# Optimization experiments

Hardware: AMD Instinct MI355X
Metric: run time of the kernel (lower is better)

The kernel has to match this reference:

```python
import jax, jax.numpy as jnp
import numpy as np

RATE = 22050.0 / 256.0  # audio_target_rate from the torch source
SIZES = [2.23147392 * RATE, 2.62519274 * RATE, 3.74199546 * RATE,
         5.78800454 * RATE, 8.02371882 * RATE, float('inf')]
WEIGHT = 1.0
EPS = 1e-7


def _giou_1d(a, b):
    # a, b: [P, 2] intervals (start, end); elementwise 1-D GIoU
    inter = jnp.clip(jnp.minimum(a[:, 1], b[:, 1]) - jnp.maximum(a[:, 0], b[:, 0]), 0.0)
    union = (a[:, 1] - a[:, 0]) + (b[:, 1] - b[:, 0]) - inter
    iou = inter / (union + EPS)
    enclose = jnp.maximum(a[:, 1], b[:, 1]) - jnp.minimum(a[:, 0], b[:, 0])
    return iou - (enclose - union) / (enclose + EPS)


def setup_inputs() -> dict:
    key = jax.random.key(0)
    ks = jax.random.split(key, 4)
    B, N = 4, 32
    L0 = 131072  # frames at the finest level
    levels = 6
    anchors = {f"anchors_l{i}": (jnp.arange(L0 >> i, dtype=jnp.float32) + 0.5) * (2.0 ** i)
               for i in range(levels)}
    A = sum(int(v.shape[0]) for v in anchors.values())  # 258048
    # GT intervals: all rows belong to class 0 (matches class_id filter in the source)
    starts = jax.random.uniform(ks[0], (B, N), minval=0.0, maxval=float(L0) - 2000.0)
    lens = jax.random.uniform(ks[1], (B, N), minval=50.0, maxval=1500.0)
    annotations = jnp.stack([starts, starts + lens, jnp.zeros((B, N))], axis=-1).astype(jnp.float32)
    # Predicted intervals for every anchor
    c = jax.random.uniform(ks[2], (B, A), minval=0.0, maxval=float(L0))
    w = jax.random.uniform(ks[3], (B, A), minval=10.0, maxval=2000.0)
    regressions = jnp.stack([c - 0.5 * w, c + 0.5 * w], axis=-1).astype(jnp.float32)
    out = {"regressions": regressions, "annotations": annotations, "class_id": 0}
    out.update(anchors)
    return out


def reference(regressions, annotations, anchors_l0, anchors_l1, anchors_l2,
              anchors_l3, anchors_l4, anchors_l5, class_id):
    anchors_list = [anchors_l0, anchors_l1, anchors_l2, anchors_l3, anchors_l4, anchors_l5]
    all_pts = jnp.concatenate(anchors_list)  # [A]

    def per_sample(reg, ann):
        # ann: [N, 3]; inputs guarantee every row has class == class_id and is valid
        order = jnp.argsort(ann[:, 1] - ann[:, 0])  # sort GT by length ascending
        ann = ann[order]
        s, e = ann[:, 0:1], ann[:, 1:2]  # [N,1]
        pos_parts, nl_parts, nr_parts = [], [], []
        for i, pts in enumerate(anchors_list):
            l = pts[None, :] - s            # [N, A_i]
            r = e - pts[None, :]            # [N, A_i]
            in_gt = (l >= 0.0) & (r >= 0.0)
            m = jnp.maximum(l, r)
            lower = SIZES[i - 1] if i > 0 else 0.0
            cand = in_gt & (m >= lower) & (m < SIZES[i])
            pos_parts.append(cand.any(axis=0))
            amax = jnp.argmax(cand, axis=0)  # first True per anchor (0 if none)
            inv = 1.0 / (2.0 ** i)           # normalize l*/r* by 2**level
            nl_parts.append(jnp.take_along_axis(l, amax[None, :], axis=0)[0] * inv)
            nr_parts.append(jnp.take_along_axis(r, amax[None, :], axis=0)[0] * inv)
        pos = jnp.concatenate(pos_parts)   # [A] bool
        nl = jnp.concatenate(nl_parts)     # [A]
        nr = jnp.concatenate(nr_parts)     # [A]
        # decoded normalized target boxes around the anchor points
        boxes = jnp.stack([all_pts - nl, all_pts + nr], axis=1)  # [A, 2]
        giou = jnp.clip(_giou_1d(boxes, reg[:, :2]), -1.0, 1.0)
        loss = 1.0 - giou
        posf = pos.astype(loss.dtype)
        # masked mean over positive anchors (torch indexes by boolean mask then .mean())
        return jnp.sum(loss * posf) / jnp.maximum(jnp.sum(posf), 1.0) * WEIGHT

    return jax.vmap(per_sample)(regressions, annotations)  # [B] per-sample losses
```

## Files before the change

kernel.cpp:

```cpp
#include <hip/hip_runtime.h>

#define EPS_F 1e-7f
#define NN 32
#define MARGIN 3
#define NSEG (NN * 6)
#define TPB 1024
#define CHUNK 4
#define CAND_MAX 24576

__global__ __launch_bounds__(TPB) void rl_fused(
    const float* __restrict__ reg,
    const float* __restrict__ ann,
    int c0, int A,
    float* __restrict__ out)
{
    const int b = blockIdx.x;
    const int t = threadIdx.x;
    const int wave = t >> 6;
    const int lane = t & 63;

    __shared__ float2 sh_se[NN];
    __shared__ int4   seg[NSEG];
    __shared__ int    pfx[NSEG];
    __shared__ unsigned segmask[NSEG];
    __shared__ unsigned cand32[CAND_MAX / 4];
    __shared__ float  sh_sz[8];
    __shared__ float  red_l[TPB / 64], red_p[TPB / 64];

    if (t < 8) {
        const float szc[8] = {
            0.0f,
            (float)(2.23147392 * (22050.0 / 256.0)),
            (float)(2.62519274 * (22050.0 / 256.0)),
            (float)(3.74199546 * (22050.0 / 256.0)),
            (float)(5.78800454 * (22050.0 / 256.0)),
            (float)(8.02371882 * (22050.0 / 256.0)),
            __builtin_inff(), __builtin_inff()
        };
        sh_sz[t] = szc[t];
    }

    if (t < NN) {
        const float* an = ann + (size_t)b * (size_t)NN * 3;
        const float s0 = an[t * 3 + 0];
        const float e0 = an[t * 3 + 1];
        const float len = e0 - s0;
        int rank = 0;
#pragma unroll
        for (int j = 0; j < NN; ++j) {
            const float lj = __shfl(len, j, 64);
            rank += (lj < len) || (lj == len && j < t);
        }
        sh_se[rank] = make_float2(s0, e0);
    }
    __syncthreads();

    float tsx, tsy;
    {
        const float2 tmp = sh_se[lane & 31];
        tsx = tmp.x; tsy = tmp.y;
    }

    if (t < NSEG) {
        const int n   = t / 6;
        const int lvl = t - n * 6;
        const float2 se = sh_se[n];
        const float s = se.x, e = se.y;
        const float mid   = 0.5f * (s + e);
        const float halfL = 0.5f * (e - s);
        const float lo = sh_sz[lvl];
        const float hi = sh_sz[lvl + 1];
        const int   cnt = c0 >> lvl;
        const float inv   = __int_as_float((127 - lvl) << 23);
        const float scale = __int_as_float((127 + lvl) << 23);

        const float dlo = fmaxf(lo - halfL, 0.0f);
        const float dhi = hi - halfL;
        const float prl = fmaxf(mid + dlo, s);
        const float prh = fminf(mid + dhi, e);
        const float pll = fmaxf(mid - dhi, s);
        const float plh = fminf(mid - dlo, e);

        int r0 = (int)floorf(prl * inv - 0.5f) - MARGIN;
        int r1 = (int)floorf(prh * inv - 0.5f) + MARGIN;
        int l0 = (int)floorf(pll * inv - 0.5f) - MARGIN;
        int l1 = (int)floorf(plh * inv - 0.5f) + MARGIN;
        r0 = max(r0, 0); r1 = min(r1, cnt - 1);
        l0 = max(l0, 0); l1 = min(l1, cnt - 1);
        if (r1 >= r0) l1 = min(l1, r0 - 1);
        const int lenL = max(l1 - l0 + 1, 0);
        const int lenR = max(r1 - r0 + 1, 0);
        seg[t] = make_int4(l0, r0, lenL | (lenR << 16), (n << 8) | lvl);
        pfx[t] = lenL + lenR;

        const int firstloc = lenL ? l0 : r0;
        const int lastloc  = lenR ? r1 : l1;
        const float ptmin = ((float)firstloc + 0.5f) * scale;
        const float ptmax = ((float)lastloc  + 0.5f) * scale;
        unsigned msk = 0u;
#pragma unroll
        for (int n2 = 0; n2 < NN - 1; ++n2) {
            const float ox = __shfl(tsx, n2, 64);
            const float oy = __shfl(tsy, n2, 64);
            msk |= ((n2 < n) & (ox <= ptmax) & (oy >= ptmin)) ? (1u << n2) : 0u;
        }
        segmask[t] = msk;
    }
    __syncthreads();

    if (wave == 0) {
        int carry = 0;
#pragma unroll
        for (int k = 0; k < 3; ++k) {
            int v = pfx[k * 64 + lane];
#pragma unroll
            for (int o = 1; o < 64; o <<= 1) {
                const int u = __shfl_up(v, o, 64);
                v += (lane >= o) ? u : 0;
            }
            pfx[k * 64 + lane] = v + carry;
            carry += __shfl(v, 63, 64);
        }
    }
    __syncthreads();
    const int T = min(pfx[NSEG - 1], CAND_MAX);

    if (t < NSEG) {
        const int4 sg = seg[t];
        const int count = (sg.z & 0xffff) + (sg.z >> 16);
        const int start = pfx[t] - count;
        seg[t].w = sg.w | (start << 16);
        unsigned char* cbw = (unsigned char*)cand32;
        int i = start;
        const int end = min(start + count, CAND_MAX);
        const unsigned rep = 0x01010101u * (unsigned)t;
        while (i < end && (i & 3)) cbw[i++] = (unsigned char)t;
        for (; i + 4 <= end; i += 4) cand32[i >> 2] = rep;
        for (; i < end; ++i) cbw[i] = (unsigned char)t;
    }
    __syncthreads();

    const int twoc0 = 2 * c0;
    const unsigned char* cb = (const unsigned char*)cand32;
    const float2* reg2 = (const float2*)reg + (size_t)b * A;
    float loss_sum = 0.0f, pos_sum = 0.0f;

    for (int jb = t; jb < T; jb += TPB * CHUNK) {
        float2 gk[CHUNK];
        float  ptk[CHUNK], lk[CHUNK], rk[CHUNK], lok[CHUNK], hik[CHUNK], invk[CHUNK];
        unsigned mskk[CHUNK];
        bool validk[CHUNK];
#pragma unroll
        for (int k = 0; k < CHUNK; ++k) {
            const int j = jb + k * TPB;
            const bool act = j < T;
            const int jj = act ? j : 0;
            const int sid = cb[jj];
            const int4 sg = seg[sid];
            mskk[k] = segmask[sid];
            const int lenL  = sg.z & 0xffff;
            const int start = (int)(((unsigned)sg.w) >> 16);
            const int n     = (sg.w >> 8) & 0xff;
            const int lvl   = sg.w & 0xff;
            const int local = jj - start;
            const int loc = (local < lenL) ? (sg.x + local) : (sg.y + (local - lenL));
            const float scale = __int_as_float((127 + lvl) << 23);
            invk[k] = __int_as_float((127 - lvl) << 23);
            const int aoff = twoc0 - (twoc0 >> lvl);

            gk[k] = reg2[aoff + loc];

            const float pt = ((float)loc + 0.5f) * scale;
            ptk[k] = pt;
            lok[k] = sh_sz[lvl];
            hik[k] = sh_sz[lvl + 1];
            const float2 se = sh_se[n];
            const float l = pt - se.x;
            const float r = se.y - pt;
            lk[k] = l; rk[k] = r;
            const float m = fmaxf(l, r);
            validk[k] = act & (fminf(l, r) >= 0.0f) & (m >= lok[k]) & (m < hik[k]);
        }

#pragma unroll
        for (int k = 0; k < CHUNK; ++k) {
            bool valid = validk[k];
            unsigned msk = mskk[k];
            const float pt = ptk[k];
            const float lo = lok[k], hi = hik[k];
            while (valid && msk) {
                const int n2 = __builtin_ctz(msk);
                msk &= msk - 1u;
                const float2 o = sh_se[n2];
                const float l2 = pt - o.x;
                const float r2 = o.y - pt;
                const float m2 = fmaxf(l2, r2);
                if ((fminf(l2, r2) >= 0.0f) & (m2 >= lo) & (m2 < hi)) valid = false;
            }

            const float inv = invk[k];
            const float2 g = gk[k];
            const float b0 = pt - lk[k] * inv;
            const float b1 = pt + rk[k] * inv;
            const float inter = fmaxf(fminf(b1, g.y) - fmaxf(b0, g.x), 0.0f);
            const float uni = (b1 - b0) + (g.y - g.x) - inter;
            const float iou = inter * __builtin_amdgcn_rcpf(uni + EPS_F);
            const float enc = fmaxf(b1, g.y) - fminf(b0, g.x);
            float giou = iou - (enc - uni) * __builtin_amdgcn_rcpf(enc + EPS_F);
            giou = fminf(fmaxf(giou, -1.0f), 1.0f);
            loss_sum += valid ? (1.0f - giou) : 0.0f;
            pos_sum  += valid ? 1.0f : 0.0f;
        }
    }

    for (int o = 32; o > 0; o >>= 1) {
        loss_sum += __shfl_down(loss_sum, o, 64);
        pos_sum  += __shfl_down(pos_sum,  o, 64);
    }
    if (lane == 0) { red_l[wave] = loss_sum; red_p[wave] = pos_sum; }
    __syncthreads();
    if (t < 16) {
        float Ls = red_l[t];
        float Ps = red_p[t];
#pragma unroll
        for (int o = 8; o > 0; o >>= 1) {
            Ls += __shfl_down(Ls, o, 16);
            Ps += __shfl_down(Ps, o, 16);
        }
        if (t == 0) out[b] = Ls / fmaxf(Ps, 1.0f);
    }
}

extern "C" void kernel_launch(void* const* d_in, const int* in_sizes, int n_in,
                              void* d_out, int out_size, void* d_ws, size_t ws_size,
                              hipStream_t stream) {
    const float* reg = (const float*)d_in[0];
    const float* ann = (const float*)d_in[1];
    const int c0 = in_sizes[3];
    const int A = in_sizes[3] + in_sizes[4] + in_sizes[5] +
                  in_sizes[6] + in_sizes[7] + in_sizes[8];
    const int B = out_size;
    (void)d_ws; (void)ws_size;

    rl_fused<<<dim3(B), TPB, 0, stream>>>(reg, ann, c0, A, (float*)d_out);
}
```

Baseline: 73.94 us.

## Split each sample across multiple blocks with atomic last-block reduction

```diff
diff --git a/kernel.cpp b/kernel.cpp
--- a/kernel.cpp
+++ b/kernel.cpp
@@ -4,17 +4,21 @@
 #define NN 32
 #define MARGIN 3
 #define NSEG (NN * 6)
-#define TPB 1024
+#define TPB 256
+#define SLICES 8
 #define CHUNK 4
 #define CAND_MAX 24576
-
-__global__ __launch_bounds__(TPB) void rl_fused(
+#define CNT_OFF 4096
+
+__global__ __launch_bounds__(TPB) void rl_sliced(
     const float* __restrict__ reg,
     const float* __restrict__ ann,
     int c0, int A,
+    float* __restrict__ ws,
     float* __restrict__ out)
 {
-    const int b = blockIdx.x;
+    const int s_blk = blockIdx.x;
+    const int b = blockIdx.y;
     const int t = threadIdx.x;
     const int wave = t >> 6;
     const int lane = t & 63;
@@ -145,14 +149,14 @@
     const float2* reg2 = (const float2*)reg + (size_t)b * A;
     float loss_sum = 0.0f, pos_sum = 0.0f;
 
-    for (int jb = t; jb < T; jb += TPB * CHUNK) {
+    for (int jb = s_blk * TPB + t; jb < T; jb += SLICES * TPB * CHUNK) {
         float2 gk[CHUNK];
         float  ptk[CHUNK], lk[CHUNK], rk[CHUNK], lok[CHUNK], hik[CHUNK], invk[CHUNK];
         unsigned mskk[CHUNK];
         bool validk[CHUNK];
 #pragma unroll
         for (int k = 0; k < CHUNK; ++k) {
-            const int j = jb + k * TPB;
+            const int j = jb + k * (SLICES * TPB);
             const bool act = j < T;
             const int jj = act ? j : 0;
             const int sid = cb[jj];
@@ -219,15 +223,28 @@
     }
     if (lane == 0) { red_l[wave] = loss_sum; red_p[wave] = pos_sum; }
     __syncthreads();
-    if (t < 16) {
-        float Ls = red_l[t];
-        float Ps = red_p[t];
-#pragma unroll
-        for (int o = 8; o > 0; o >>= 1) {
-            Ls += __shfl_down(Ls, o, 16);
-            Ps += __shfl_down(Ps, o, 16);
-        }
-        if (t == 0) out[b] = Ls / fmaxf(Ps, 1.0f);
+
+    if (t == 0) {
+        float Ls = 0.0f, Ps = 0.0f;
+#pragma unroll
+        for (int w = 0; w < TPB / 64; ++w) { Ls += red_l[w]; Ps += red_p[w]; }
+        float* slot = ws + ((size_t)b * SLICES + s_blk) * 2;
+        atomicExch(&slot[0], Ls);
+        atomicExch(&slot[1], Ps);
+        __threadfence();
+        unsigned* cnt = (unsigned*)((char*)ws + CNT_OFF + (size_t)b * 64);
+        const unsigned old = atomicAdd(cnt, 1u);
+        if (old == SLICES - 1) {
+            __threadfence();
+            float Lt = 0.0f, Pt = 0.0f;
+#pragma unroll
+            for (int i = 0; i < SLICES; ++i) {
+                float* sl = ws + ((size_t)b * SLICES + i) * 2;
+                Lt += atomicAdd(&sl[0], 0.0f);
+                Pt += atomicAdd(&sl[1], 0.0f);
+            }
+            out[b] = Lt / fmaxf(Pt, 1.0f);
+        }
     }
 }
 
@@ -240,7 +257,8 @@
     const int A = in_sizes[3] + in_sizes[4] + in_sizes[5] +
                   in_sizes[6] + in_sizes[7] + in_sizes[8];
     const int B = out_size;
-    (void)d_ws; (void)ws_size;
-
-    rl_fused<<<dim3(B), TPB, 0, stream>>>(reg, ann, c0, A, (float*)d_out);
+
+    hipMemsetAsync(d_ws, 0, 8192, stream);
+    rl_sliced<<<dim3(SLICES, B), TPB, 0, stream>>>(
+        reg, ann, c0, A, (float*)d_ws, (float*)d_out);
 }
```

New measurement: 83.42 us. 12.8% more time.

## Assign one half-wave per GT interval, dropping prefix-scan candidate list

Applied to the files above, without the earlier changes.

```diff
diff --git a/kernel.cpp b/kernel.cpp
--- a/kernel.cpp
+++ b/kernel.cpp
@@ -3,12 +3,10 @@
 #define EPS_F 1e-7f
 #define NN 32
 #define MARGIN 3
-#define NSEG (NN * 6)
 #define TPB 1024
-#define CHUNK 4
-#define CAND_MAX 24576
-
-__global__ __launch_bounds__(TPB) void rl_fused(
+#define CHUNK 2
+
+__global__ __launch_bounds__(TPB) void rl_lean(
     const float* __restrict__ reg,
     const float* __restrict__ ann,
     int c0, int A,
@@ -18,12 +16,10 @@
     const int t = threadIdx.x;
     const int wave = t >> 6;
     const int lane = t & 63;
+    const int n    = t >> 5;
+    const int slot = t & 31;
 
     __shared__ float2 sh_se[NN];
-    __shared__ int4   seg[NSEG];
-    __shared__ int    pfx[NSEG];
-    __shared__ unsigned segmask[NSEG];
-    __shared__ unsigned cand32[CAND_MAX / 4];
     __shared__ float  sh_sz[8];
     __shared__ float  red_l[TPB / 64], red_p[TPB / 64];
 
@@ -55,128 +51,96 @@
     }
     __syncthreads();
 
+    const float2 myse = sh_se[n];
+    const float s = myse.x, e = myse.y;
     float tsx, tsy;
     {
         const float2 tmp = sh_se[lane & 31];
         tsx = tmp.x; tsy = tmp.y;
     }
 
-    if (t < NSEG) {
-        const int n   = t / 6;
-        const int lvl = t - n * 6;
-        const float2 se = sh_se[n];
-        const float s = se.x, e = se.y;
-        const float mid   = 0.5f * (s + e);
-        const float halfL = 0.5f * (e - s);
-        const float lo = sh_sz[lvl];
-        const float hi = sh_sz[lvl + 1];
-        const int   cnt = c0 >> lvl;
-        const float inv   = __int_as_float((127 - lvl) << 23);
-        const float scale = __int_as_float((127 + lvl) << 23);
-
-        const float dlo = fmaxf(lo - halfL, 0.0f);
-        const float dhi = hi - halfL;
-        const float prl = fmaxf(mid + dlo, s);
-        const float prh = fminf(mid + dhi, e);
-        const float pll = fmaxf(mid - dhi, s);
-        const float plh = fminf(mid - dlo, e);
-
-        int r0 = (int)floorf(prl * inv - 0.5f) - MARGIN;
-        int r1 = (int)floorf(prh * inv - 0.5f) + MARGIN;
-        int l0 = (int)floorf(pll * inv - 0.5f) - MARGIN;
-        int l1 = (int)floorf(plh * inv - 0.5f) + MARGIN;
-        r0 = max(r0, 0); r1 = min(r1, cnt - 1);
-        l0 = max(l0, 0); l1 = min(l1, cnt - 1);
-        if (r1 >= r0) l1 = min(l1, r0 - 1);
-        const int lenL = max(l1 - l0 + 1, 0);
-        const int lenR = max(r1 - r0 + 1, 0);
-        seg[t] = make_int4(l0, r0, lenL | (lenR << 16), (n << 8) | lvl);
-        pfx[t] = lenL + lenR;
-
-        const int firstloc = lenL ? l0 : r0;
-        const int lastloc  = lenR ? r1 : l1;
-        const float ptmin = ((float)firstloc + 0.5f) * scale;
-        const float ptmax = ((float)lastloc  + 0.5f) * scale;
-        unsigned msk = 0u;
-#pragma unroll
-        for (int n2 = 0; n2 < NN - 1; ++n2) {
-            const float ox = __shfl(tsx, n2, 64);
-            const float oy = __shfl(tsy, n2, 64);
-            msk |= ((n2 < n) & (ox <= ptmax) & (oy >= ptmin)) ? (1u << n2) : 0u;
-        }
-        segmask[t] = msk;
-    }
-    __syncthreads();
-
-    if (wave == 0) {
-        int carry = 0;
-#pragma unroll
-        for (int k = 0; k < 3; ++k) {
-            int v = pfx[k * 64 + lane];
-#pragma unroll
-            for (int o = 1; o < 64; o <<= 1) {
-                const int u = __shfl_up(v, o, 64);
-                v += (lane >= o) ? u : 0;
-            }
-            pfx[k * 64 + lane] = v + carry;
-            carry += __shfl(v, 63, 64);
-        }
-    }
-    __syncthreads();
-    const int T = min(pfx[NSEG - 1], CAND_MAX);
-
-    if (t < NSEG) {
-        const int4 sg = seg[t];
-        const int count = (sg.z & 0xffff) + (sg.z >> 16);
-        const int start = pfx[t] - count;
-        seg[t].w = sg.w | (start << 16);
-        unsigned char* cbw = (unsigned char*)cand32;
-        int i = start;
-        const int end = min(start + count, CAND_MAX);
-        const unsigned rep = 0x01010101u * (unsigned)t;
-        while (i < end && (i & 3)) cbw[i++] = (unsigned char)t;
-        for (; i + 4 <= end; i += 4) cand32[i >> 2] = rep;
-        for (; i < end; ++i) cbw[i] = (unsigned char)t;
-    }
-    __syncthreads();
+    unsigned msk_gt = 0u;
+#pragma unroll
+    for (int n2 = 0; n2 < NN - 1; ++n2) {
+        const float ox = __shfl(tsx, n2, 64);
+        const float oy = __shfl(tsy, n2, 64);
+        msk_gt |= ((n2 < n) & (ox <= e) & (oy >= s)) ? (1u << n2) : 0u;
+    }
+
+    const float mid   = 0.5f * (s + e);
+    const float halfL = 0.5f * (e - s);
+    int l0a[6], r0a[6], lenLa[6], cumi[6];
+    {
+        int run = 0;
+#pragma unroll
+        for (int lvl = 0; lvl < 6; ++lvl) {
+            const float lo = sh_sz[lvl];
+            const float hi = sh_sz[lvl + 1];
+            const int   cnt = c0 >> lvl;
+            const float inv = __int_as_float((127 - lvl) << 23);
+
+            const float dlo = fmaxf(lo - halfL, 0.0f);
+            const float dhi = hi - halfL;
+            const float prl = fmaxf(mid + dlo, s);
+            const float prh = fminf(mid + dhi, e);
+            const float pll = fmaxf(mid - dhi, s);
+            const float plh = fminf(mid - dlo, e);
+
+            int r0 = (int)floorf(prl * inv - 0.5f) - MARGIN;
+            int r1 = (int)floorf(prh * inv - 0.5f) + MARGIN;
+            int l0 = (int)floorf(pll * inv - 0.5f) - MARGIN;
+            int l1 = (int)floorf(plh * inv - 0.5f) + MARGIN;
+            r0 = max(r0, 0); r1 = min(r1, cnt - 1);
+            l0 = max(l0, 0); l1 = min(l1, cnt - 1);
+            if (r1 >= r0) l1 = min(l1, r0 - 1);
+            const int lenL = max(l1 - l0 + 1, 0);
+            const int lenR = max(r1 - r0 + 1, 0);
+            l0a[lvl] = l0; r0a[lvl] = r0; lenLa[lvl] = lenL;
+            run += lenL + lenR;
+            cumi[lvl] = run;
+        }
+    }
+    const int total = cumi[5];
 
     const int twoc0 = 2 * c0;
-    const unsigned char* cb = (const unsigned char*)cand32;
     const float2* reg2 = (const float2*)reg + (size_t)b * A;
     float loss_sum = 0.0f, pos_sum = 0.0f;
 
-    for (int jb = t; jb < T; jb += TPB * CHUNK) {
+    for (int cb = slot; cb < total; cb += 32 * CHUNK) {
         float2 gk[CHUNK];
         float  ptk[CHUNK], lk[CHUNK], rk[CHUNK], lok[CHUNK], hik[CHUNK], invk[CHUNK];
-        unsigned mskk[CHUNK];
         bool validk[CHUNK];
 #pragma unroll
         for (int k = 0; k < CHUNK; ++k) {
-            const int j = jb + k * TPB;
-            const bool act = j < T;
-            const int jj = act ? j : 0;
-            const int sid = cb[jj];
-            const int4 sg = seg[sid];
-            mskk[k] = segmask[sid];
-            const int lenL  = sg.z & 0xffff;
-            const int start = (int)(((unsigned)sg.w) >> 16);
-            const int n     = (sg.w >> 8) & 0xff;
-            const int lvl   = sg.w & 0xff;
-            const int local = jj - start;
-            const int loc = (local < lenL) ? (sg.x + local) : (sg.y + (local - lenL));
-            const float scale = __int_as_float((127 + lvl) << 23);
-            invk[k] = __int_as_float((127 - lvl) << 23);
-            const int aoff = twoc0 - (twoc0 >> lvl);
+            const int c = cb + k * 32;
+            const bool act = c < total;
+            const int cc = act ? c : cb;
+
+            int base = 0, pl0 = l0a[0], pr0 = r0a[0], plenL = lenLa[0], plvl = 0;
+#pragma unroll
+            for (int L = 1; L < 6; ++L) {
+                const bool sel = cc >= cumi[L - 1];
+                base  = sel ? cumi[L - 1] : base;
+                pl0   = sel ? l0a[L]   : pl0;
+                pr0   = sel ? r0a[L]   : pr0;
+                plenL = sel ? lenLa[L] : plenL;
+                plvl  = sel ? L        : plvl;
+            }
+            const int local = cc - base;
+            const int loc = (local < plenL) ? (pl0 + local)
+                                            : (pr0 + (local - plenL));
+            const float scale = __int_as_float((127 + plvl) << 23);
+            invk[k] = __int_as_float((127 - plvl) << 23);
+            const int aoff = twoc0 - (twoc0 >> plvl);
 
             gk[k] = reg2[aoff + loc];
 
             const float pt = ((float)loc + 0.5f) * scale;
             ptk[k] = pt;
-            lok[k] = sh_sz[lvl];
-            hik[k] = sh_sz[lvl + 1];
-            const float2 se = sh_se[n];
-            const float l = pt - se.x;
-            const float r = se.y - pt;
+            lok[k] = sh_sz[plvl];
+            hik[k] = sh_sz[plvl + 1];
+            const float l = pt - s;
+            const float r = e - pt;
             lk[k] = l; rk[k] = r;
             const float m = fmaxf(l, r);
             validk[k] = act & (fminf(l, r) >= 0.0f) & (m >= lok[k]) & (m < hik[k]);
@@ -185,7 +149,7 @@
 #pragma unroll
         for (int k = 0; k < CHUNK; ++k) {
             bool valid = validk[k];
-            unsigned msk = mskk[k];
+            unsigned msk = msk_gt;
             const float pt = ptk[k];
             const float lo = lok[k], hi = hik[k];
             while (valid && msk) {
@@ -242,5 +206,5 @@
     const int B = out_size;
     (void)d_ws; (void)ws_size;
 
-    rl_fused<<<dim3(B), TPB, 0, stream>>>(reg, ann, c0, A, (float*)d_out);
+    rl_lean<<<dim3(B), TPB, 0, stream>>>(reg, ann, c0, A, (float*)d_out);
 }
```

New measurement: 77.18 us. 4.4% more time.
